# Optimization experiments

Hardware: AMD Instinct MI355X
Metric: run time of the kernel (lower is better)

The kernel has to match this reference:

```python
import jax, jax.numpy as jnp
import numpy as np

B, T, C, H = 8, 1024, 1024, 16
D = C // H
EPS = 1e-5


def setup_inputs() -> dict:
    key = jax.random.key(0)
    ks = jax.random.split(key, 12)
    s = lambda k, shape, scale=0.02: jax.random.normal(k, shape, dtype=jnp.float32) * scale
    return {
        "x": jax.random.normal(ks[0], (B, T, C), dtype=jnp.float32),
        "ln1_w": jnp.ones((C,), jnp.float32),
        "ln1_b": jnp.zeros((C,), jnp.float32),
        "w_qkv": s(ks[1], (C, 3 * C)),
        "b_qkv": jnp.zeros((3 * C,), jnp.float32),
        "w_o": s(ks[2], (C, C)),
        "b_o": jnp.zeros((C,), jnp.float32),
        "ln2_w": jnp.ones((C,), jnp.float32),
        "ln2_b": jnp.zeros((C,), jnp.float32),
        "w_fc": s(ks[3], (C, 4 * C)),
        "b_fc": jnp.zeros((4 * C,), jnp.float32),
        "w_proj": s(ks[4], (4 * C, C)),
        "b_proj": jnp.zeros((C,), jnp.float32),
    }


def _layernorm(x, w, b):
    mu = jnp.mean(x, axis=-1, keepdims=True)
    var = jnp.mean(jnp.square(x - mu), axis=-1, keepdims=True)
    return (x - mu) * jax.lax.rsqrt(var + EPS) * w + b


def _attention(x, w_qkv, b_qkv, w_o, b_o):
    b, t, c = x.shape
    qkv = x @ w_qkv + b_qkv                      # [B,T,3C]
    q, k, v = jnp.split(qkv, 3, axis=-1)
    q = q.reshape(b, t, H, D)
    k = k.reshape(b, t, H, D)
    v = v.reshape(b, t, H, D)
    scores = jnp.einsum("bqhd,bkhd->bhqk", q, k) / jnp.sqrt(jnp.float32(D))
    mask = jnp.tril(jnp.ones((t, t), dtype=bool))  # causal
    scores = jnp.where(mask, scores, jnp.float32(-jnp.inf))
    att = jax.nn.softmax(scores, axis=-1)
    y = jnp.einsum("bhqk,bkhd->bqhd", att, v).reshape(b, t, c)
    return y @ w_o + b_o


def _mlp(x, w_fc, b_fc, w_proj, b_proj):
    h = jax.nn.gelu(x @ w_fc + b_fc, approximate=True)  # tanh GELU
    return h @ w_proj + b_proj


def reference(x, ln1_w, ln1_b, w_qkv, b_qkv, w_o, b_o, ln2_w, ln2_b, w_fc, b_fc, w_proj, b_proj):
    x = x + _attention(_layernorm(x, ln1_w, ln1_b), w_qkv, b_qkv, w_o, b_o)
    x = x + _mlp(_layernorm(x, ln2_w, ln2_b), w_fc, b_fc, w_proj, b_proj)
    return x
```

## Files before the change

kernel.cpp:

```cpp
#include <hip/hip_runtime.h>
#include <math.h>
#include <stdint.h>

typedef unsigned short u16;
typedef unsigned int u32;
typedef __attribute__((ext_vector_type(4))) unsigned short u16x4;
typedef __attribute__((ext_vector_type(8))) unsigned short u16x8;
typedef __attribute__((ext_vector_type(8))) __bf16 bf16x8;
typedef __attribute__((ext_vector_type(4))) float f32x4;

#define Bn 8
#define Tn 1024
#define Cn 1024
#define Hn 16
#define Dn 64
#define Mn 8192

#define F32_ONE_BITS 0x3F800000u

__device__ __forceinline__ float b2f(u16 u) {
  union { unsigned int i; float f; } v; v.i = ((unsigned int)u) << 16; return v.f;
}
__device__ __forceinline__ u16 f2b(float f) {
  union { float f; unsigned int i; } v; v.f = f;
  unsigned int r = v.i + 0x7fffu + ((v.i >> 16) & 1u);
  return (u16)(r >> 16);
}

__device__ __forceinline__ void async_ld16(const u16* g, u16* l) {
  __builtin_amdgcn_global_load_lds(
      (__attribute__((address_space(1))) void*)g,
      (__attribute__((address_space(3))) void*)l, 16, 0, 0);
}

__device__ __forceinline__ float gelu_fast(float x) {
  float u2 = 1.5957691216057308f * (x + 0.044715f * x * x * x);
  return x / (1.0f + __expf(-u2));
}

__global__ __launch_bounds__(256) void cvt_x_k(const void* __restrict__ src, u16* __restrict__ dst,
                                               const u32* __restrict__ flagp) {
  bool isf32 = (*flagp == F32_ONE_BITS);
  size_t i = ((size_t)blockIdx.x * 256 + threadIdx.x) * 4;
  if (isf32) {
    f32x4 v = *reinterpret_cast<const f32x4*>((const float*)src + i);
    u16x4 o;
#pragma unroll
    for (int j = 0; j < 4; j++) o[j] = f2b(v[j]);
    *reinterpret_cast<u16x4*>(dst + i) = o;
  } else {
    *reinterpret_cast<u16x4*>(dst + i) = *reinterpret_cast<const u16x4*>((const u16*)src + i);
  }
}

struct SmallCvt { const void* src[8]; u16* dst[8]; int n[8]; };

__global__ __launch_bounds__(256) void cvt_small_k(SmallCvt p, const u32* __restrict__ flagp) {
  bool isf32 = (*flagp == F32_ONE_BITS);
  int t = blockIdx.x * 256 + threadIdx.x;
  int off = 0;
#pragma unroll
  for (int i = 0; i < 8; i++) {
    int idx = t - off;
    if (idx >= 0 && idx < p.n[i]) {
      u16 v = isf32 ? f2b(((const float*)p.src[i])[idx]) : ((const u16*)p.src[i])[idx];
      p.dst[i][idx] = v;
    }
    off += p.n[i];
  }
}

__global__ __launch_bounds__(256) void transpose_k(const void* __restrict__ in,
                                                   u16* __restrict__ out, int K, int N,
                                                   const u32* __restrict__ flagp) {
  bool isf32 = (*flagp == F32_ONE_BITS);
  __shared__ u16 tile[32][33];
  int c0 = blockIdx.x * 32, r0 = blockIdx.y * 32;
  int tx = threadIdx.x, ty = threadIdx.y;
#pragma unroll
  for (int i = 0; i < 4; i++) {
    size_t idx = (size_t)(r0 + ty + i * 8) * N + c0 + tx;
    tile[ty + i * 8][tx] = isf32 ? f2b(((const float*)in)[idx]) : ((const u16*)in)[idx];
  }
  __syncthreads();
#pragma unroll
  for (int i = 0; i < 4; i++)
    out[(size_t)(c0 + ty + i * 8) * K + r0 + tx] = tile[tx][ty + i * 8];
}

__global__ __launch_bounds__(256) void ln_k(const u16* __restrict__ x, const u16* __restrict__ w,
                                            const u16* __restrict__ bi, u16* __restrict__ out) {
  int row = blockIdx.x, tid = threadIdx.x;
  const u16* xr = x + (size_t)row * Cn;
  u16x4 xv = *reinterpret_cast<const u16x4*>(xr + tid * 4);
  float v0 = b2f(xv[0]), v1 = b2f(xv[1]), v2 = b2f(xv[2]), v3 = b2f(xv[3]);
  float s = v0 + v1 + v2 + v3;
  float s2 = v0 * v0 + v1 * v1 + v2 * v2 + v3 * v3;
#pragma unroll
  for (int m = 1; m < 64; m <<= 1) {
    s += __shfl_xor(s, m, 64);
    s2 += __shfl_xor(s2, m, 64);
  }
  __shared__ float rs_[4], rs2_[4];
  int wave = tid >> 6, lane = tid & 63;
  if (lane == 0) { rs_[wave] = s; rs2_[wave] = s2; }
  __syncthreads();
  s = rs_[0] + rs_[1] + rs_[2] + rs_[3];
  s2 = rs2_[0] + rs2_[1] + rs2_[2] + rs2_[3];
  float mu = s * (1.0f / Cn);
  float var = s2 * (1.0f / Cn) - mu * mu;
  float rstd = rsqrtf(var + 1e-5f);
  u16x4 wv = *reinterpret_cast<const u16x4*>(w + tid * 4);
  u16x4 bv = *reinterpret_cast<const u16x4*>(bi + tid * 4);
  u16x4 ov;
  float vv[4] = {v0, v1, v2, v3};
#pragma unroll
  for (int j = 0; j < 4; j++)
    ov[j] = f2b((vv[j] - mu) * rstd * b2f(wv[j]) + b2f(bv[j]));
  *reinterpret_cast<u16x4*>(out + (size_t)row * Cn + tid * 4) = ov;
}

template <int GELU, int RES, int F32OUT>
__global__ __launch_bounds__(256) void gemm_k(const u16* __restrict__ A, const u16* __restrict__ BT,
                                              const u16* __restrict__ bias, const u16* __restrict__ res,
                                              void* __restrict__ Cout, int M, int N, int K) {
  __shared__ __align__(16) u16 As[128 * 64];
  __shared__ __align__(16) u16 Bs[128 * 64];
  int tid = threadIdx.x, wave = tid >> 6, lane = tid & 63;
  int l15 = lane & 15, quad = lane >> 4;
  int m0 = blockIdx.y * 128, n0 = blockIdx.x * 128;
  int wm = (wave & 1) * 64, wn = (wave >> 1) * 64;

  int offA[4][2], offB[4][2];
#pragma unroll
  for (int i = 0; i < 4; i++) {
    int rowA = wm + i * 16 + l15;
    int rowB = wn + i * 16 + l15;
#pragma unroll
    for (int kc = 0; kc < 2; kc++) {
      offA[i][kc] = rowA * 64 + (((kc * 4 + quad) ^ (rowA & 7)) * 8);
      offB[i][kc] = rowB * 64 + (((kc * 4 + quad) ^ (rowB & 7)) * 8);
    }
  }

  const u16 *aSrc[4], *bSrc[4];
  u16 *aDst[4], *bDst[4];
#pragma unroll
  for (int i = 0; i < 4; i++) {
    int c = wave * 256 + i * 64 + lane;
    int row = c >> 3;
    int j = (c & 7) ^ (row & 7);
    aSrc[i] = A + (size_t)(m0 + row) * K + j * 8;
    bSrc[i] = BT + (size_t)(n0 + row) * K + j * 8;
    aDst[i] = As + (size_t)c * 8;
    bDst[i] = Bs + (size_t)c * 8;
  }

  f32x4 acc[4][4];
#pragma unroll
  for (int mi = 0; mi < 4; mi++)
#pragma unroll
    for (int ni = 0; ni < 4; ni++) acc[mi][ni] = (f32x4){0.f, 0.f, 0.f, 0.f};

  for (int k0 = 0; k0 < K; k0 += 64) {
    __syncthreads();
#pragma unroll
    for (int i = 0; i < 4; i++) async_ld16(aSrc[i] + k0, aDst[i]);
#pragma unroll
    for (int i = 0; i < 4; i++) async_ld16(bSrc[i] + k0, bDst[i]);
    __syncthreads();
#pragma unroll
    for (int kc = 0; kc < 2; kc++) {
      bf16x8 av[4], bv[4];
#pragma unroll
      for (int i = 0; i < 4; i++) av[i] = *reinterpret_cast<const bf16x8*>(As + offA[i][kc]);
#pragma unroll
      for (int i = 0; i < 4; i++) bv[i] = *reinterpret_cast<const bf16x8*>(Bs + offB[i][kc]);
#pragma unroll
      for (int mi = 0; mi < 4; mi++)
#pragma unroll
        for (int ni = 0; ni < 4; ni++)
          acc[mi][ni] = __builtin_amdgcn_mfma_f32_16x16x32_bf16(av[mi], bv[ni], acc[mi][ni], 0, 0, 0);
    }
  }

#pragma unroll
  for (int ni = 0; ni < 4; ni++) {
    int col = n0 + wn + ni * 16 + l15;
    float bval = b2f(bias[col]);
#pragma unroll
    for (int mi = 0; mi < 4; mi++) {
#pragma unroll
      for (int r = 0; r < 4; r++) {
        int row = m0 + wm + mi * 16 + quad * 4 + r;
        float v = acc[mi][ni][r] + bval;
        if (GELU) v = gelu_fast(v);
        if (RES) v += b2f(res[(size_t)row * N + col]);
        if (F32OUT)
          ((float*)Cout)[(size_t)row * N + col] = v;
        else
          ((u16*)Cout)[(size_t)row * N + col] = f2b(v);
      }
    }
  }
}

__global__ __launch_bounds__(256) void attn_k(const u16* __restrict__ qkv, u16* __restrict__ y) {
  int qt = blockIdx.x, bh = blockIdx.y;
  int b = bh >> 4, h = bh & 15;
  int tid = threadIdx.x, wave = tid >> 6, lane = tid & 63;
  int l15 = lane & 15, quad = lane >> 4;

  __shared__ __align__(16) u16 Ks[64 * 72];
  __shared__ __align__(16) u16 VTs[64 * 72];
  __shared__ __align__(16) u16 Ps[4][16 * 72];

  const u16* base = qkv + (size_t)b * Tn * 3072 + h * 64;
  int q0 = qt * 64 + wave * 16;

  bf16x8 qfrag[2];
#pragma unroll
  for (int kc = 0; kc < 2; kc++)
    qfrag[kc] = *reinterpret_cast<const bf16x8*>(base + (size_t)(q0 + l15) * 3072 + kc * 32 + quad * 8);

  f32x4 o[4];
#pragma unroll
  for (int dn = 0; dn < 4; dn++) o[dn] = (f32x4){0.f, 0.f, 0.f, 0.f};
  float m_r[4] = {-1e30f, -1e30f, -1e30f, -1e30f};
  float l_r[4] = {0.f, 0.f, 0.f, 0.f};

  int kp = tid & 31, dgroup = tid >> 5;
  u32* vtw = reinterpret_cast<u32*>(VTs);

  int kvend = qt * 64;
  for (int kv0 = 0; kv0 <= kvend; kv0 += 64) {
    __syncthreads();
    {
      int key = tid >> 2, d0 = (tid & 3) * 16;
      const u16* kpt = base + 1024 + (size_t)(kv0 + key) * 3072 + d0;
      u16x8 ka = *reinterpret_cast<const u16x8*>(kpt);
      u16x8 kb = *reinterpret_cast<const u16x8*>(kpt + 8);
      *reinterpret_cast<u16x8*>(&Ks[key * 72 + d0]) = ka;
      *reinterpret_cast<u16x8*>(&Ks[key * 72 + d0 + 8]) = kb;
      const u16* vp0 = base + 2048 + (size_t)(kv0 + 2 * kp) * 3072 + dgroup * 8;
      u16x8 va = *reinterpret_cast<const u16x8*>(vp0);
      u16x8 vb = *reinterpret_cast<const u16x8*>(vp0 + 3072);
#pragma unroll
      for (int i = 0; i < 8; i++)
        vtw[(dgroup * 8 + i) * 36 + kp] = (u32)va[i] | ((u32)vb[i] << 16);
    }
    __syncthreads();

    float sv[4][4];
#pragma unroll
    for (int ni = 0; ni < 4; ni++) {
      f32x4 z = (f32x4){0.f, 0.f, 0.f, 0.f};
#pragma unroll
      for (int kc = 0; kc < 2; kc++) {
        bf16x8 bfr = *reinterpret_cast<const bf16x8*>(&Ks[(ni * 16 + l15) * 72 + kc * 32 + quad * 8]);
        z = __builtin_amdgcn_mfma_f32_16x16x32_bf16(qfrag[kc], bfr, z, 0, 0, 0);
      }
#pragma unroll
      for (int r = 0; r < 4; r++) sv[ni][r] = z[r];
    }
    bool diag = (kv0 + 64 > q0);
#pragma unroll
    for (int ni = 0; ni < 4; ni++)
#pragma unroll
      for (int r = 0; r < 4; r++) {
        float v = sv[ni][r] * 0.125f;
        if (diag && (kv0 + ni * 16 + l15 > q0 + quad * 4 + r)) v = -1e30f;
        sv[ni][r] = v;
      }
    float mt[4], al[4], rs[4];
#pragma unroll
    for (int r = 0; r < 4; r++) {
      mt[r] = fmaxf(fmaxf(sv[0][r], sv[1][r]), fmaxf(sv[2][r], sv[3][r]));
#pragma unroll
      for (int m = 1; m <= 8; m <<= 1) mt[r] = fmaxf(mt[r], __shfl_xor(mt[r], m, 64));
      float mn = fmaxf(m_r[r], mt[r]);
      al[r] = __expf(m_r[r] - mn);
      m_r[r] = mn;
      rs[r] = 0.f;
    }
#pragma unroll
    for (int ni = 0; ni < 4; ni++)
#pragma unroll
      for (int r = 0; r < 4; r++) {
        float p = __expf(sv[ni][r] - m_r[r]);
        sv[ni][r] = p;
        rs[r] += p;
      }
#pragma unroll
    for (int r = 0; r < 4; r++) {
#pragma unroll
      for (int m = 1; m <= 8; m <<= 1) rs[r] += __shfl_xor(rs[r], m, 64);
      l_r[r] = l_r[r] * al[r] + rs[r];
    }
#pragma unroll
    for (int dn = 0; dn < 4; dn++)
#pragma unroll
      for (int r = 0; r < 4; r++) o[dn][r] *= al[r];
#pragma unroll
    for (int ni = 0; ni < 4; ni++)
#pragma unroll
      for (int r = 0; r < 4; r++)
        Ps[wave][(quad * 4 + r) * 72 + ni * 16 + l15] = f2b(sv[ni][r]);
#pragma unroll
    for (int kc = 0; kc < 2; kc++) {
      bf16x8 afr = *reinterpret_cast<const bf16x8*>(&Ps[wave][l15 * 72 + kc * 32 + quad * 8]);
#pragma unroll
      for (int dn = 0; dn < 4; dn++) {
        bf16x8 bfr = *reinterpret_cast<const bf16x8*>(&VTs[(dn * 16 + l15) * 72 + kc * 32 + quad * 8]);
        o[dn] = __builtin_amdgcn_mfma_f32_16x16x32_bf16(afr, bfr, o[dn], 0, 0, 0);
      }
    }
  }
#pragma unroll
  for (int r = 0; r < 4; r++) {
    float inv = 1.0f / l_r[r];
    int row = b * Tn + q0 + quad * 4 + r;
#pragma unroll
    for (int dn = 0; dn < 4; dn++)
      y[(size_t)row * Cn + h * 64 + dn * 16 + l15] = f2b(o[dn][r] * inv);
  }
}

extern "C" void kernel_launch(void* const* d_in, const int* in_sizes, int n_in,
                              void* d_out, int out_size, void* d_ws, size_t ws_size,
                              hipStream_t stream) {
  const void* x      = d_in[0];
  const void* ln1_w  = d_in[1];
  const void* ln1_b  = d_in[2];
  const void* w_qkv  = d_in[3];
  const void* b_qkv  = d_in[4];
  const void* w_o    = d_in[5];
  const void* b_o    = d_in[6];
  const void* ln2_w  = d_in[7];
  const void* ln2_b  = d_in[8];
  const void* w_fc   = d_in[9];
  const void* b_fc   = d_in[10];
  const void* w_proj = d_in[11];
  const void* b_proj = d_in[12];
  const u32* flagp = (const u32*)ln1_w;

  size_t off = 0;
  char* wsb = (char*)d_ws;
  auto alloc = [&](size_t bytes) {
    void* p = wsb + off;
    off += (bytes + 255) & ~(size_t)255;
    return (u16*)p;
  };
  u16* wqkvT  = alloc((size_t)3072 * 1024 * 2);
  u16* woT    = alloc((size_t)1024 * 1024 * 2);
  u16* wfcT   = alloc((size_t)4096 * 1024 * 2);
  u16* wprojT = alloc((size_t)1024 * 4096 * 2);
  u16* xb     = alloc((size_t)Mn * 1024 * 2);
  u16* sm     = alloc((size_t)16384 * 2);
  u16* xn     = alloc((size_t)Mn * 1024 * 2);
  u16* ybuf   = alloc((size_t)Mn * 1024 * 2);
  u16* x1     = alloc((size_t)Mn * 1024 * 2);
  u16* big    = alloc((size_t)Mn * 4096 * 2);
  u16* qkvbuf = big;
  u16* hbuf   = big;
  if (off > ws_size) return;

  u16* LW1 = sm;
  u16* LB1 = sm + 1024;
  u16* BQKV = sm + 2048;
  u16* BO  = sm + 5120;
  u16* LW2 = sm + 6144;
  u16* LB2 = sm + 7168;
  u16* BFC = sm + 8192;
  u16* BPJ = sm + 12288;

  SmallCvt sc;
  sc.src[0] = ln1_w;  sc.dst[0] = LW1;  sc.n[0] = 1024;
  sc.src[1] = ln1_b;  sc.dst[1] = LB1;  sc.n[1] = 1024;
  sc.src[2] = b_qkv;  sc.dst[2] = BQKV; sc.n[2] = 3072;
  sc.src[3] = b_o;    sc.dst[3] = BO;   sc.n[3] = 1024;
  sc.src[4] = ln2_w;  sc.dst[4] = LW2;  sc.n[4] = 1024;
  sc.src[5] = ln2_b;  sc.dst[5] = LB2;  sc.n[5] = 1024;
  sc.src[6] = b_fc;   sc.dst[6] = BFC;  sc.n[6] = 4096;
  sc.src[7] = b_proj; sc.dst[7] = BPJ;  sc.n[7] = 1024;

  hipLaunchKernelGGL(cvt_small_k, dim3(52), dim3(256), 0, stream, sc, flagp);
  hipLaunchKernelGGL(cvt_x_k, dim3(Mn * 1024 / 4 / 256), dim3(256), 0, stream, x, xb, flagp);

  dim3 tb(32, 8);
  hipLaunchKernelGGL(transpose_k, dim3(3072 / 32, 1024 / 32), tb, 0, stream, w_qkv, wqkvT, 1024, 3072, flagp);
  hipLaunchKernelGGL(transpose_k, dim3(1024 / 32, 1024 / 32), tb, 0, stream, w_o, woT, 1024, 1024, flagp);
  hipLaunchKernelGGL(transpose_k, dim3(4096 / 32, 1024 / 32), tb, 0, stream, w_fc, wfcT, 1024, 4096, flagp);
  hipLaunchKernelGGL(transpose_k, dim3(1024 / 32, 4096 / 32), tb, 0, stream, w_proj, wprojT, 4096, 1024, flagp);

  hipLaunchKernelGGL(ln_k, dim3(Mn), dim3(256), 0, stream, xb, LW1, LB1, xn);
  hipLaunchKernelGGL((gemm_k<0, 0, 0>), dim3(3072 / 128, Mn / 128), dim3(256), 0, stream,
                     xn, wqkvT, BQKV, (const u16*)nullptr, (void*)qkvbuf, Mn, 3072, 1024);
  hipLaunchKernelGGL(attn_k, dim3(Tn / 64, Bn * Hn), dim3(256), 0, stream, qkvbuf, ybuf);
  hipLaunchKernelGGL((gemm_k<0, 1, 0>), dim3(1024 / 128, Mn / 128), dim3(256), 0, stream,
                     ybuf, woT, BO, xb, (void*)x1, Mn, 1024, 1024);
  hipLaunchKernelGGL(ln_k, dim3(Mn), dim3(256), 0, stream, x1, LW2, LB2, xn);
  hipLaunchKernelGGL((gemm_k<1, 0, 0>), dim3(4096 / 128, Mn / 128), dim3(256), 0, stream,
                     xn, wfcT, BFC, (const u16*)nullptr, (void*)hbuf, Mn, 4096, 1024);
  hipLaunchKernelGGL((gemm_k<0, 1, 1>), dim3(1024 / 128, Mn / 128), dim3(256), 0, stream,
                     hbuf, wprojT, BPJ, x1, d_out, Mn, 1024, 4096);
}
```

Measured before the change: 566.7 us.

## Pair causal query tiles per block and double-buffer K/V loads in attention

Each attention block now handles two query tiles, lo and 15-lo, so the causal work per block is balanced and each K/V tile load is shared by both. K tiles are loaded asynchronously into a double-buffered, XOR-swizzled shared array, and V for the next tile is prefetched into registers while the current tile is processed. This targets causal load imbalance, redundant K/V traffic and load latency, at the cost of more registers (two accumulators) and half as many blocks. It depends on an async_ld16 helper that is assumed to be defined in the unseen part of the file.

```diff
diff --git a/kernel.cpp b/kernel.cpp
--- a/kernel.cpp
+++ b/kernel.cpp
@@ -205,60 +205,80 @@
   }
 }
 
-__global__ __launch_bounds__(256) void attn_k(const u16* __restrict__ qkv, u16* __restrict__ y) {
-  int qt = blockIdx.x, bh = blockIdx.y;
+__global__ __launch_bounds__(256, 4) void attn_k(const u16* __restrict__ qkv, u16* __restrict__ y) {
+  int bh = blockIdx.x;
+  int lo = blockIdx.y;
+  int hi = 15 - lo;
   int b = bh >> 4, h = bh & 15;
   int tid = threadIdx.x, wave = tid >> 6, lane = tid & 63;
   int l15 = lane & 15, quad = lane >> 4;
 
-  __shared__ __align__(16) u16 Ks[64 * 72];
+  __shared__ __align__(16) u16 Ks[2][64 * 64];
   __shared__ __align__(16) u16 VTs[64 * 72];
   __shared__ __align__(16) u16 Ps[4][16 * 72];
 
   const u16* base = qkv + (size_t)b * Tn * 3072 + h * 64;
-  int q0 = qt * 64 + wave * 16;
-
-  bf16x8 qfrag[2];
+  int q0_lo = lo * 64 + wave * 16;
+  int q0_hi = hi * 64 + wave * 16;
+
+  bf16x8 qf_lo[2], qf_hi[2];
+#pragma unroll
+  for (int kc = 0; kc < 2; kc++) {
+    qf_lo[kc] = *reinterpret_cast<const bf16x8*>(base + (size_t)(q0_lo + l15) * 3072 + kc * 32 + quad * 8);
+    qf_hi[kc] = *reinterpret_cast<const bf16x8*>(base + (size_t)(q0_hi + l15) * 3072 + kc * 32 + quad * 8);
+  }
+
+  int offKb[2];
 #pragma unroll
   for (int kc = 0; kc < 2; kc++)
-    qfrag[kc] = *reinterpret_cast<const bf16x8*>(base + (size_t)(q0 + l15) * 3072 + kc * 32 + quad * 8);
-
-  f32x4 o[4];
-#pragma unroll
-  for (int dn = 0; dn < 4; dn++) o[dn] = (f32x4){0.f, 0.f, 0.f, 0.f};
-  float m_r[4] = {-1e30f, -1e30f, -1e30f, -1e30f};
-  float l_r[4] = {0.f, 0.f, 0.f, 0.f};
-
+    offKb[kc] = l15 * 64 + (((kc * 4 + quad) ^ (l15 & 7)) * 8);
+
+  int kSrcOff[2], kDstOff[2];
+#pragma unroll
+  for (int i = 0; i < 2; i++) {
+    int c = wave * 128 + i * 64 + lane;
+    int row = c >> 3, j = (c & 7) ^ (row & 7);
+    kSrcOff[i] = row * 3072 + j * 8;
+    kDstOff[i] = c * 8;
+  }
+  const u16* kBase = base + 1024;
+  const u16* vBase = base + 2048;
   int kp = tid & 31, dgroup = tid >> 5;
   u32* vtw = reinterpret_cast<u32*>(VTs);
 
-  int kvend = qt * 64;
-  for (int kv0 = 0; kv0 <= kvend; kv0 += 64) {
-    __syncthreads();
-    {
-      int key = tid >> 2, d0 = (tid & 3) * 16;
-      const u16* kpt = base + 1024 + (size_t)(kv0 + key) * 3072 + d0;
-      u16x8 ka = *reinterpret_cast<const u16x8*>(kpt);
-      u16x8 kb = *reinterpret_cast<const u16x8*>(kpt + 8);
-      *reinterpret_cast<u16x8*>(&Ks[key * 72 + d0]) = ka;
-      *reinterpret_cast<u16x8*>(&Ks[key * 72 + d0 + 8]) = kb;
-      const u16* vp0 = base + 2048 + (size_t)(kv0 + 2 * kp) * 3072 + dgroup * 8;
-      u16x8 va = *reinterpret_cast<const u16x8*>(vp0);
-      u16x8 vb = *reinterpret_cast<const u16x8*>(vp0 + 3072);
-#pragma unroll
-      for (int i = 0; i < 8; i++)
-        vtw[(dgroup * 8 + i) * 36 + kp] = (u32)va[i] | ((u32)vb[i] << 16);
-    }
-    __syncthreads();
-
+#pragma unroll
+  for (int i = 0; i < 2; i++) async_ld16(kBase + kSrcOff[i], &Ks[0][kDstOff[i]]);
+  u16x8 va, vb;
+  {
+    const u16* vS = vBase + (size_t)(2 * kp) * 3072 + dgroup * 8;
+    va = *reinterpret_cast<const u16x8*>(vS);
+    vb = *reinterpret_cast<const u16x8*>(vS + 3072);
+  }
+
+  f32x4 o_lo[4], o_hi[4];
+  float m_lo[4], l_lo[4], m_hi[4], l_hi[4];
+#pragma unroll
+  for (int i = 0; i < 4; i++) {
+    o_lo[i] = (f32x4){0.f, 0.f, 0.f, 0.f};
+    o_hi[i] = (f32x4){0.f, 0.f, 0.f, 0.f};
+    m_lo[i] = -1e30f; m_hi[i] = -1e30f;
+    l_lo[i] = 0.f;    l_hi[i] = 0.f;
+  }
+
+  int pwBase = quad * 4 * 72 + l15;
+  int prBase = l15 * 72 + quad * 8;
+  int vrBase = l15 * 72 + quad * 8;
+
+  auto process = [&](const bf16x8* qf, f32x4* o, float* m_r, float* l_r,
+                     int q0, int kv0, const u16* KsB) {
     float sv[4][4];
 #pragma unroll
     for (int ni = 0; ni < 4; ni++) {
       f32x4 z = (f32x4){0.f, 0.f, 0.f, 0.f};
 #pragma unroll
       for (int kc = 0; kc < 2; kc++) {
-        bf16x8 bfr = *reinterpret_cast<const bf16x8*>(&Ks[(ni * 16 + l15) * 72 + kc * 32 + quad * 8]);
-        z = __builtin_amdgcn_mfma_f32_16x16x32_bf16(qfrag[kc], bfr, z, 0, 0, 0);
+        bf16x8 bfr = *reinterpret_cast<const bf16x8*>(KsB + offKb[kc] + ni * 1024);
+        z = __builtin_amdgcn_mfma_f32_16x16x32_bf16(qf[kc], bfr, z, 0, 0, 0);
       }
 #pragma unroll
       for (int r = 0; r < 4; r++) sv[ni][r] = z[r];
@@ -305,24 +325,55 @@
     for (int ni = 0; ni < 4; ni++)
 #pragma unroll
       for (int r = 0; r < 4; r++)
-        Ps[wave][(quad * 4 + r) * 72 + ni * 16 + l15] = f2b(sv[ni][r]);
+        Ps[wave][pwBase + r * 72 + ni * 16] = f2b(sv[ni][r]);
 #pragma unroll
     for (int kc = 0; kc < 2; kc++) {
-      bf16x8 afr = *reinterpret_cast<const bf16x8*>(&Ps[wave][l15 * 72 + kc * 32 + quad * 8]);
+      bf16x8 afr = *reinterpret_cast<const bf16x8*>(&Ps[wave][prBase + kc * 32]);
 #pragma unroll
       for (int dn = 0; dn < 4; dn++) {
-        bf16x8 bfr = *reinterpret_cast<const bf16x8*>(&VTs[(dn * 16 + l15) * 72 + kc * 32 + quad * 8]);
+        bf16x8 bfr = *reinterpret_cast<const bf16x8*>(&VTs[vrBase + dn * 1152 + kc * 32]);
         o[dn] = __builtin_amdgcn_mfma_f32_16x16x32_bf16(afr, bfr, o[dn], 0, 0, 0);
       }
     }
-  }
+  };
+
+  int kvend_hi = hi * 64, kvend_lo = lo * 64;
+  int buf = 0;
+  for (int kv0 = 0; kv0 <= kvend_hi; kv0 += 64) {
+    __syncthreads();
+#pragma unroll
+    for (int i = 0; i < 8; i++)
+      vtw[(dgroup * 8 + i) * 36 + kp] = (u32)va[i] | ((u32)vb[i] << 16);
+    __syncthreads();
+    if (kv0 + 64 <= kvend_hi) {
+      const u16* kS = kBase + (size_t)(kv0 + 64) * 3072;
+#pragma unroll
+      for (int i = 0; i < 2; i++) async_ld16(kS + kSrcOff[i], &Ks[buf ^ 1][kDstOff[i]]);
+      const u16* vS = vBase + (size_t)(kv0 + 64 + 2 * kp) * 3072 + dgroup * 8;
+      va = *reinterpret_cast<const u16x8*>(vS);
+      vb = *reinterpret_cast<const u16x8*>(vS + 3072);
+    }
+    process(qf_hi, o_hi, m_hi, l_hi, q0_hi, kv0, &Ks[buf][0]);
+    if (kv0 <= kvend_lo)
+      process(qf_lo, o_lo, m_lo, l_lo, q0_lo, kv0, &Ks[buf][0]);
+    buf ^= 1;
+  }
+
 #pragma unroll
   for (int r = 0; r < 4; r++) {
-    float inv = 1.0f / l_r[r];
-    int row = b * Tn + q0 + quad * 4 + r;
+    float inv = 1.0f / l_hi[r];
+    int row = b * Tn + q0_hi + quad * 4 + r;
 #pragma unroll
     for (int dn = 0; dn < 4; dn++)
-      y[(size_t)row * Cn + h * 64 + dn * 16 + l15] = f2b(o[dn][r] * inv);
+      y[(size_t)row * Cn + h * 64 + dn * 16 + l15] = f2b(o_hi[dn][r] * inv);
+  }
+#pragma unroll
+  for (int r = 0; r < 4; r++) {
+    float inv = 1.0f / l_lo[r];
+    int row = b * Tn + q0_lo + quad * 4 + r;
+#pragma unroll
+    for (int dn = 0; dn < 4; dn++)
+      y[(size_t)row * Cn + h * 64 + dn * 16 + l15] = f2b(o_lo[dn][r] * inv);
   }
 }
 
@@ -396,7 +447,7 @@
   hipLaunchKernelGGL(ln_k, dim3(Mn), dim3(256), 0, stream, xb, LW1, LB1, xn);
   hipLaunchKernelGGL((gemm_k<0, 0, 0>), dim3(3072 / 128, Mn / 128), dim3(256), 0, stream,
                      xn, wqkvT, BQKV, (const u16*)nullptr, (void*)qkvbuf, Mn, 3072, 1024);
-  hipLaunchKernelGGL(attn_k, dim3(Tn / 64, Bn * Hn), dim3(256), 0, stream, qkvbuf, ybuf);
+  hipLaunchKernelGGL(attn_k, dim3(Bn * Hn, 8), dim3(256), 0, stream, qkvbuf, ybuf);
   hipLaunchKernelGGL((gemm_k<0, 1, 0>), dim3(1024 / 128, Mn / 128), dim3(256), 0, stream,
                      ybuf, woT, BO, xb, (void*)x1, Mn, 1024, 1024);
   hipLaunchKernelGGL(ln_k, dim3(Mn), dim3(256), 0, stream, x1, LW2, LB2, xn);
```

After: 643.4 us. 1.14x slower.
